# Performance work log

Measured on AMD Instinct MI355X. Metric: run time of the kernel, lower is better.

Reference implementation:

```python
import jax, jax.numpy as jnp
import numpy as np

# --- Cl(3,0,1) projective geometric algebra structure constants (GATr blade order) ---
BLADES = [(), (0,), (1,), (2,), (3,), (0, 1), (0, 2), (0, 3), (1, 2), (1, 3), (2, 3),
          (0, 1, 2), (0, 1, 3), (0, 2, 3), (1, 2, 3), (0, 1, 2, 3)]
IDX = {b: i for i, b in enumerate(BLADES)}
METRIC = [0.0, 1.0, 1.0, 1.0]  # e0 degenerate, e1,e2,e3 square to +1


def _mul_blades(a, b):
    """Multiply two basis blades; returns (sign, sorted_blade_tuple)."""
    lst = list(a) + list(b)
    sign = 1.0
    changed = True
    while changed:
        changed = False
        k = 0
        while k < len(lst) - 1:
            if lst[k] > lst[k + 1]:
                lst[k], lst[k + 1] = lst[k + 1], lst[k]
                sign = -sign
                changed = True
            elif lst[k] == lst[k + 1]:
                sign *= METRIC[lst[k]]
                del lst[k:k + 2]
                changed = True
            else:
                k += 1
    return sign, tuple(lst)


def _tables():
    gp = np.zeros((16, 16, 16), np.float32)
    outer = np.zeros((16, 16, 16), np.float32)
    for j, bj in enumerate(BLADES):
        for k, bk in enumerate(BLADES):
            s, bl = _mul_blades(bj, bk)
            if s != 0.0:
                gp[IDX[bl], j, k] = s
            if set(bj).isdisjoint(bk):  # outer product: nonzero only for disjoint blades
                outer[IDX[bl], j, k] = s
    # dual map D: blade -> signed complement, with blade ^ complement = sign * e0123
    D = np.zeros((16, 16), np.float32)
    for j, bj in enumerate(BLADES):
        comp = tuple(i for i in range(4) if i not in bj)
        s, _ = _mul_blades(bj, comp)
        D[IDX[comp], j] = s
    # join(x, y) = dual(dual(x) ^ dual(y))  ->  bilinear tensor [16,16,16]
    join = np.einsum('ai,ijk,jb,kc->abc', D, outer, D, D).astype(np.float32)
    # Pin-equivariant linear basis: 5 grade projections + 4 e0-wedge-per-grade maps
    grades = np.array([len(b) for b in BLADES])
    basis = np.zeros((9, 16, 16), np.float32)
    for g in range(5):
        basis[g] = np.diag((grades == g).astype(np.float32))
    e0_mul = outer[:, IDX[(0,)], :]  # x -> e0 ^ x
    for g in range(4):
        basis[5 + g] = e0_mul * (grades == g)[None, :].astype(np.float32)
    return gp, join, basis


B, N = 8, 4096
IN_MV, HID, OUT_MV = 32, 32, 32
HALF = HID // 2
IN_S, OUT_S = 64, 64
NB = 9


def setup_inputs() -> dict:
    key = jax.random.key(0)
    ks = jax.random.split(key, 16)
    gp, jn, basis = _tables()

    def wmv(k, o, i):
        return jax.random.normal(k, (o, i, NB), jnp.float32) / np.sqrt(i * NB)

    def ws(k, o, i):
        return jax.random.normal(k, (o, i), jnp.float32) / np.sqrt(i)

    return dict(
        multivectors=jax.random.normal(ks[0], (B, N, IN_MV, 16), jnp.float32),
        reference_mv=jax.random.normal(ks[1], (B, N, 16), jnp.float32),
        scalars=jax.random.normal(ks[2], (B, N, IN_S), jnp.float32),
        basis=jnp.asarray(basis), gp=jnp.asarray(gp), jn=jnp.asarray(jn),
        w_left_mv=wmv(ks[3], HALF, IN_MV), w_left_s=ws(ks[4], HALF, IN_S),
        w_right_mv=wmv(ks[5], HALF, IN_MV), w_right_s=ws(ks[6], HALF, IN_S),
        w_jl_mv=wmv(ks[7], HALF, IN_MV), w_jl_s=ws(ks[8], HALF, IN_S),
        w_jr_mv=wmv(ks[9], HALF, IN_MV), w_jr_s=ws(ks[10], HALF, IN_S),
        w_out_mv=wmv(ks[11], OUT_MV, HID), w_out_s2mv=ws(ks[12], OUT_MV, IN_S),
        w_out_mvs2s=ws(ks[13], OUT_S, HID), w_out_s2s=ws(ks[14], OUT_S, IN_S),
    )


def _equi_linear(x, s, w_mv, w_s, basis):
    # fold the 9 equivariant basis maps into the channel-mixing weight once (tiny)
    W = jnp.einsum('oib,bjk->oijk', w_mv, basis)  # [out, in, 16, 16]
    out = jnp.einsum('oijk,...ik->...oj', W, x)   # (..., out, 16)
    # scalar inputs feed the multivector scalar component (blade index 0)
    out = out.at[..., 0].add(jnp.einsum('os,...s->...o', w_s, s))
    return out


def reference(multivectors, reference_mv, scalars, basis, gp, jn,
              w_left_mv, w_left_s, w_right_mv, w_right_s, w_jl_mv, w_jl_s,
              w_jr_mv, w_jr_s, w_out_mv, w_out_s2mv, w_out_mvs2s, w_out_s2s):
    left = _equi_linear(multivectors, scalars, w_left_mv, w_left_s, basis)
    right = _equi_linear(multivectors, scalars, w_right_mv, w_right_s, basis)
    gp_out = jnp.einsum('ijk,...cj,...ck->...ci', gp, left, right)  # geometric product

    jl = _equi_linear(multivectors, scalars, w_jl_mv, w_jl_s, basis)
    jr = _equi_linear(multivectors, scalars, w_jr_mv, w_jr_s, basis)
    # equivariant join, scaled by pseudoscalar (e0123) component of the reference
    join_out = jnp.einsum('ijk,...cj,...ck->...ci', jn, jl, jr) * reference_mv[..., None, 15:16]

    hidden = jnp.concatenate([gp_out, join_out], axis=-2)  # (..., HID, 16)
    out_mv = _equi_linear(hidden, scalars, w_out_mv, w_out_s2mv, basis)
    out_s = jnp.einsum('oc,...c->...o', w_out_mvs2s, hidden[..., 0]) \
        + jnp.einsum('os,...s->...o', w_out_s2s, scalars)
    return out_mv, out_s
```

## Files before the change

### kernel.cpp

```cpp
#include <hip/hip_runtime.h>
#include <stdint.h>


#define NPOS_TOTAL 32768

typedef __attribute__((ext_vector_type(8))) short short8;
typedef __attribute__((ext_vector_type(4))) float f32x4;
#define MFMA16(a,b,c) __builtin_amdgcn_mfma_f32_16x16x32_bf16((a),(b),(c),0,0,0)

constexpr int BLADE_MASK[16] = {0,1,2,4,8,3,5,9,6,10,12,7,11,13,14,15};
constexpr int MASK2IDX[16]   = {0,1,2,5,3,6,8,11,4,7,9,12,10,13,14,15};

struct MulRes { int sign; int mask; };

constexpr MulRes mul_blades(int ma, int mb) {
  int lst[8] = {0,0,0,0,0,0,0,0};
  int n = 0;
  for (int g = 0; g < 4; ++g) if ((ma >> g) & 1) lst[n++] = g;
  for (int g = 0; g < 4; ++g) if ((mb >> g) & 1) lst[n++] = g;
  int sign = 1;
  bool changed = true;
  while (changed) {
    changed = false;
    int k = 0;
    while (k + 1 < n) {
      if (lst[k] > lst[k+1]) {
        int t = lst[k]; lst[k] = lst[k+1]; lst[k+1] = t;
        sign = -sign; changed = true;
      } else if (lst[k] == lst[k+1]) {
        if (lst[k] == 0) sign = 0;
        for (int m = k; m + 2 < n; ++m) lst[m] = lst[m+2];
        n -= 2; changed = true;
      } else {
        ++k;
      }
    }
  }
  int mask = 0;
  for (int m = 0; m < n; ++m) mask |= (1 << lst[m]);
  if (sign == 0) mask = 0;
  return MulRes{sign, mask};
}

struct Tables {
  float gp_sgn[16][16]; int gp_idx[16][16];
  float jn_sgn[16][16]; int jn_idx[16][16];
  constexpr Tables() : gp_sgn{}, gp_idx{}, jn_sgn{}, jn_idx{} {
    for (int j = 0; j < 16; ++j) {
      for (int k = 0; k < 16; ++k) {
        MulRes r = mul_blades(BLADE_MASK[j], BLADE_MASK[k]);
        gp_sgn[j][k] = (float)r.sign;
        gp_idx[j][k] = MASK2IDX[r.mask & 15];
        jn_sgn[j][k] = 0.0f; jn_idx[j][k] = 0;
        int mb = BLADE_MASK[j], mc = BLADE_MASK[k];
        if ((mb | mc) == 15) {
          int cb = 15 ^ mb, cc = 15 ^ mc;
          MulRes sb = mul_blades(mb, cb);
          MulRes sc = mul_blades(mc, cc);
          MulRes ro = mul_blades(cb, cc);
          int imask = ro.mask;
          int amask = 15 ^ imask;
          MulRes si = mul_blades(imask, amask);
          jn_sgn[j][k] = (float)(si.sign * ro.sign * sb.sign * sc.sign);
          jn_idx[j][k] = MASK2IDX[amask & 15];
        }
      }
    }
  }
};
constexpr Tables TBL{};

constexpr int GRADE[16] = {0,1,1,1,1,2,2,2,2,2,2,3,3,3,3,4};
constexpr int E0_TGT[8]  = {1,5,6,7,11,12,13,15};
constexpr int E0_SRC[8]  = {0,2,3,4,8,9,10,14};
constexpr int E0_SLOT[8] = {5,6,6,6,7,7,7,8};

__device__ __forceinline__ float bflo(unsigned u) { return __uint_as_float(u << 16); }
__device__ __forceinline__ float bfhi(unsigned u) { return __uint_as_float(u & 0xffff0000u); }
__device__ __forceinline__ unsigned pk2(float a, float b) {
  unsigned ua = __float_as_uint(a), ub = __float_as_uint(b);
  unsigned ra = (ua + 0x7fffu + ((ua >> 16) & 1u)) >> 16;
  unsigned rb = (ub + 0x7fffu + ((ub >> 16) & 1u)) >> 16;
  return (ra & 0xffffu) | ((rb & 0xffffu) << 16);
}
__device__ __forceinline__ unsigned short bf1(float a) {
  unsigned ua = __float_as_uint(a);
  return (unsigned short)((ua + 0x7fffu + ((ua >> 16) & 1u)) >> 16);
}

__global__ void gb_prep(const float* __restrict__ wlmv, const float* __restrict__ wrmv,
                        const float* __restrict__ wjlmv, const float* __restrict__ wjrmv,
                        const float* __restrict__ wls,  const float* __restrict__ wrs,
                        const float* __restrict__ wjls, const float* __restrict__ wjrs,
                        const float* __restrict__ womv, const float* __restrict__ ws2mv,
                        const float* __restrict__ wm2s, const float* __restrict__ ws2s,
                        uint4* __restrict__ wpk) {
  int t = blockIdx.x * 256 + threadIdx.x;
  if (t >= 168 * 64) return;
  int blk = t >> 6, l = t & 63;
  int m = l & 15, q = l >> 4;
  float v[8];
  if (blk < 104) {
    int mat = blk >> 2, ot = blk & 3;
    const float* wmv[4] = {wlmv, wrmv, wjlmv, wjrmv};
    const float* wsc[4] = {wls, wrs, wjls, wjrs};
    for (int jj = 0; jj < 8; ++jj) {
      int k = q * 8 + jj;
      if (mat < 16)      v[jj] = wmv[ot][m * 288 + k * 9 + GRADE[mat]];
      else if (mat < 24) v[jj] = wmv[ot][m * 288 + k * 9 + E0_SLOT[mat - 16]];
      else               v[jj] = wsc[ot][m * 64 + (mat - 24) * 32 + k];
    }
  } else if (blk < 156) {
    int b2 = blk - 104, mat = b2 >> 1, ot = b2 & 1;
    int o = ot * 16 + m;
    for (int jj = 0; jj < 8; ++jj) {
      int k = q * 8 + jj;
      if (mat < 16)      v[jj] = womv[o * 288 + k * 9 + GRADE[mat]];
      else if (mat < 24) v[jj] = womv[o * 288 + k * 9 + E0_SLOT[mat - 16]];
      else               v[jj] = ws2mv[o * 64 + (mat - 24) * 32 + k];
    }
  } else {
    int b4 = blk - 156;
    for (int jj = 0; jj < 8; ++jj) {
      int k = q * 8 + jj;
      if (b4 < 4) { int o = b4 * 16 + m; v[jj] = wm2s[o * 32 + k]; }
      else { int half = (b4 - 4) >> 2, ot = (b4 - 4) & 3; int o = ot * 16 + m;
             v[jj] = ws2s[o * 64 + half * 32 + k]; }
    }
  }
  uint4 u;
  u.x = pk2(v[0], v[1]); u.y = pk2(v[2], v[3]);
  u.z = pk2(v[4], v[5]); u.w = pk2(v[6], v[7]);
  wpk[t] = u;
}

__global__ __launch_bounds__(256, 4) void gb_main(
    const float* __restrict__ mv, const float* __restrict__ ref,
    const float* __restrict__ s, const uint4* __restrict__ wpk,
    float* __restrict__ out_mv, float* __restrict__ out_s) {
  __shared__ __align__(16) char smem[37376];
  unsigned short* xs_e = (unsigned short*)smem;
  unsigned*       xs_w = (unsigned*)smem;
  unsigned short* hl_e = (unsigned short*)smem;
  unsigned*       yl_w = (unsigned*)smem;

  const int tid  = threadIdx.x;
  const int wave = tid >> 6, lane = tid & 63;
  const int lm = lane & 15, lq = lane >> 4;
  const int P0 = blockIdx.x * 16;

  const float rs = ref[((size_t)(P0 + (tid & 15))) * 16 + 15];

  const float4* mv4 = (const float4*)mv + (size_t)P0 * 128;
  #pragma unroll
  for (int kk = 0; kk < 4; ++kk) {
    int e = tid + kk * 256;
    int p = e >> 6, sub = e & 63, i2 = sub >> 2, jg = sub & 3;
    float4 fa = mv4[p * 128 + i2 * 8 + jg];
    float4 fb = mv4[p * 128 + i2 * 8 + 4 + jg];
    int base = p * 260 + jg * 4 * 16 + i2;
    xs_w[base + 0 * 16] = pk2(fa.x, fb.x);
    xs_w[base + 1 * 16] = pk2(fa.y, fb.y);
    xs_w[base + 2 * 16] = pk2(fa.z, fb.z);
    xs_w[base + 3 * 16] = pk2(fa.w, fb.w);
  }

  short8 sfrag[2];
  {
    const float4* s4 = (const float4*)s + ((size_t)(P0 + lm)) * 16;
    #pragma unroll
    for (int h = 0; h < 2; ++h) {
      float4 a = s4[h * 8 + lq * 2];
      float4 b = s4[h * 8 + lq * 2 + 1];
      uint4 u;
      u.x = pk2(a.x, a.y); u.y = pk2(a.z, a.w);
      u.z = pk2(b.x, b.y); u.w = pk2(b.z, b.w);
      sfrag[h] = __builtin_bit_cast(short8, u);
    }
  }
  __syncthreads();

  {
    short8 bx[16];
    #pragma unroll
    for (int c = 0; c < 16; ++c)
      bx[c] = *(const short8*)&xs_e[lm * 520 + c * 32 + lq * 8];
    __syncthreads();
    f32x4 zf = {0.f, 0.f, 0.f, 0.f};
    f32x4 acc[16];
    #pragma unroll
    for (int j = 0; j < 16; ++j) acc[j] = zf;
    #pragma unroll
    for (int j = 0; j < 16; ++j) {
      short8 w = __builtin_bit_cast(short8, wpk[(j * 4 + wave) * 64 + lane]);
      acc[j] = MFMA16(w, bx[j], acc[j]);
    }
    #pragma unroll
    for (int m = 0; m < 8; ++m) {
      short8 w = __builtin_bit_cast(short8, wpk[((16 + m) * 4 + wave) * 64 + lane]);
      acc[E0_TGT[m]] = MFMA16(w, bx[E0_SRC[m]], acc[E0_TGT[m]]);
    }
    #pragma unroll
    for (int h = 0; h < 2; ++h) {
      short8 w = __builtin_bit_cast(short8, wpk[((24 + h) * 4 + wave) * 64 + lane]);
      acc[0] = MFMA16(w, sfrag[h], acc[0]);
    }
    #pragma unroll
    for (int jp = 0; jp < 8; ++jp) {
      #pragma unroll
      for (int r = 0; r < 4; ++r) {
        int o = wave * 16 + lq * 4 + r;
        yl_w[o * 146 + lm * 9 + jp] = pk2(acc[2 * jp][r], acc[2 * jp + 1][r]);
      }
    }
  }
  __syncthreads();

  {
    const int pos = tid & 15;
    const int hc  = tid >> 4;
    unsigned uL[8], uR[8];
    {
      const unsigned* pL = yl_w + hc * 146 + pos * 9;
      const unsigned* pR = yl_w + (16 + hc) * 146 + pos * 9;
      #pragma unroll
      for (int q = 0; q < 8; ++q) uL[q] = pL[q];
      #pragma unroll
      for (int q = 0; q < 8; ++q) uR[q] = pR[q];
    }
    __syncthreads();
    float L[16], R[16], H[16];
    #pragma unroll
    for (int q = 0; q < 8; ++q) {
      L[2*q] = bflo(uL[q]); L[2*q+1] = bfhi(uL[q]);
      R[2*q] = bflo(uR[q]); R[2*q+1] = bfhi(uR[q]);
    }
    #pragma unroll
    for (int q = 0; q < 16; ++q) H[q] = 0.f;
    #pragma unroll
    for (int j = 0; j < 16; ++j)
      #pragma unroll
      for (int k = 0; k < 16; ++k)
        if (TBL.gp_sgn[j][k] != 0.0f)
          H[TBL.gp_idx[j][k]] += TBL.gp_sgn[j][k] * L[j] * R[k];
    #pragma unroll
    for (int j = 0; j < 16; ++j)
      hl_e[pos * 520 + j * 32 + hc] = bf1(H[j]);
    {
      const unsigned* pJ = yl_w + (32 + hc) * 146 + pos * 9;
      const unsigned* pK = yl_w + (48 + hc) * 146 + pos * 9;
      #pragma unroll
      for (int q = 0; q < 8; ++q) {
        unsigned a = pJ[q];
        L[2*q] = bflo(a) * rs; L[2*q+1] = bfhi(a) * rs;
      }
      #pragma unroll
      for (int q = 0; q < 8; ++q) {
        unsigned a = pK[q];
        R[2*q] = bflo(a); R[2*q+1] = bfhi(a);
      }
    }
    #pragma unroll
    for (int q = 0; q < 16; ++q) H[q] = 0.f;
    #pragma unroll
    for (int j = 0; j < 16; ++j)
      #pragma unroll
      for (int k = 0; k < 16; ++k)
        if (TBL.jn_sgn[j][k] != 0.0f)
          H[TBL.jn_idx[j][k]] += TBL.jn_sgn[j][k] * L[j] * R[k];
    #pragma unroll
    for (int j = 0; j < 16; ++j)
      hl_e[pos * 520 + j * 32 + 16 + hc] = bf1(H[j]);
  }
  __syncthreads();

  if (wave < 2) {
    short8 bh[16];
    #pragma unroll
    for (int j = 0; j < 16; ++j)
      bh[j] = *(const short8*)&hl_e[lm * 520 + j * 32 + lq * 8];
    f32x4 zf = {0.f, 0.f, 0.f, 0.f};
    f32x4 a3[16];
    #pragma unroll
    for (int j = 0; j < 16; ++j) a3[j] = zf;
    #pragma unroll
    for (int j = 0; j < 16; ++j) {
      short8 w = __builtin_bit_cast(short8, wpk[(104 + j * 2 + wave) * 64 + lane]);
      a3[j] = MFMA16(w, bh[j], a3[j]);
    }
    #pragma unroll
    for (int m = 0; m < 8; ++m) {
      short8 w = __builtin_bit_cast(short8, wpk[(104 + (16 + m) * 2 + wave) * 64 + lane]);
      a3[E0_TGT[m]] = MFMA16(w, bh[E0_SRC[m]], a3[E0_TGT[m]]);
    }
    #pragma unroll
    for (int h = 0; h < 2; ++h) {
      short8 w = __builtin_bit_cast(short8, wpk[(104 + (24 + h) * 2 + wave) * 64 + lane]);
      a3[0] = MFMA16(w, sfrag[h], a3[0]);
    }
    float* ob = out_mv + ((size_t)(P0 + lm)) * 512 + (size_t)(wave * 16 + lq * 4) * 16;
    #pragma unroll
    for (int r = 0; r < 4; ++r) {
      #pragma unroll
      for (int g = 0; g < 4; ++g) {
        *(float4*)(ob + r * 16 + g * 4) =
            make_float4(a3[4*g][r], a3[4*g+1][r], a3[4*g+2][r], a3[4*g+3][r]);
      }
    }
  } else {
    short8 bh0 = *(const short8*)&hl_e[lm * 520 + lq * 8];
    int w2 = wave - 2;
    f32x4 zf = {0.f, 0.f, 0.f, 0.f};
    #pragma unroll
    for (int t2 = 0; t2 < 2; ++t2) {
      int otg = w2 * 2 + t2;
      f32x4 aS = zf;
      aS = MFMA16(__builtin_bit_cast(short8, wpk[(156 + otg) * 64 + lane]), bh0, aS);
      aS = MFMA16(__builtin_bit_cast(short8, wpk[(160 + otg) * 64 + lane]), sfrag[0], aS);
      aS = MFMA16(__builtin_bit_cast(short8, wpk[(164 + otg) * 64 + lane]), sfrag[1], aS);
      float* osb = out_s + ((size_t)(P0 + lm)) * 64 + otg * 16 + lq * 4;
      *(float4*)osb = make_float4(aS[0], aS[1], aS[2], aS[3]);
    }
  }
}

extern "C" void kernel_launch(void* const* d_in, const int* in_sizes, int n_in,
                              void* d_out, int out_size, void* d_ws, size_t ws_size,
                              hipStream_t stream) {
  (void)in_sizes; (void)n_in; (void)out_size; (void)ws_size;
  const float* mv    = (const float*)d_in[0];
  const float* ref   = (const float*)d_in[1];
  const float* s     = (const float*)d_in[2];
  const float* wlmv  = (const float*)d_in[6];
  const float* wls   = (const float*)d_in[7];
  const float* wrmv  = (const float*)d_in[8];
  const float* wrs   = (const float*)d_in[9];
  const float* wjlmv = (const float*)d_in[10];
  const float* wjls  = (const float*)d_in[11];
  const float* wjrmv = (const float*)d_in[12];
  const float* wjrs  = (const float*)d_in[13];
  const float* womv  = (const float*)d_in[14];
  const float* ws2mv = (const float*)d_in[15];
  const float* wm2s  = (const float*)d_in[16];
  const float* ws2s  = (const float*)d_in[17];

  float* out_mv = (float*)d_out;
  float* out_s  = out_mv + (size_t)NPOS_TOTAL * 32 * 16;
  uint4* wpk = (uint4*)d_ws;

  gb_prep<<<42, 256, 0, stream>>>(wlmv, wrmv, wjlmv, wjrmv, wls, wrs, wjls, wjrs,
                                  womv, ws2mv, wm2s, ws2s, wpk);
  gb_main<<<NPOS_TOTAL / 16, 256, 0, stream>>>(mv, ref, s, wpk, out_mv, out_s);
}
```

Baseline: 194.6 us.

## Deduplicate packed weights by grade slot and prefetch them early, separating LDS regions

The weight packing stores one fragment per unique grade/e0 slot (9 per operand) instead of one per blade, which shrinks the packed weight buffer. The main kernel loads these fragments into registers at kernel start and before the final barrier, so their latency overlaps the input staging. The y buffer moves to its own LDS region, which lets two __syncthreads be removed. In exchange, LDS use grows and launch bounds drop to 2 blocks per CU, which may lower occupancy and raise register pressure.

```diff
diff --git a/kernel.cpp b/kernel.cpp
--- a/kernel.cpp
+++ b/kernel.cpp
@@ -96,36 +96,50 @@
                         const float* __restrict__ wm2s, const float* __restrict__ ws2s,
                         uint4* __restrict__ wpk) {
   int t = blockIdx.x * 256 + threadIdx.x;
-  if (t >= 168 * 64) return;
+  if (t >= 78 * 64) return;
   int blk = t >> 6, l = t & 63;
   int m = l & 15, q = l >> 4;
   float v[8];
-  if (blk < 104) {
-    int mat = blk >> 2, ot = blk & 3;
+  if (blk < 36) {
+    int slot = blk >> 2, ot = blk & 3;
     const float* wmv[4] = {wlmv, wrmv, wjlmv, wjrmv};
+    for (int jj = 0; jj < 8; ++jj) {
+      int k = q * 8 + jj;
+      v[jj] = wmv[ot][m * 288 + k * 9 + slot];
+    }
+  } else if (blk < 44) {
+    int b = blk - 36, h = b >> 2, ot = b & 3;
     const float* wsc[4] = {wls, wrs, wjls, wjrs};
     for (int jj = 0; jj < 8; ++jj) {
       int k = q * 8 + jj;
-      if (mat < 16)      v[jj] = wmv[ot][m * 288 + k * 9 + GRADE[mat]];
-      else if (mat < 24) v[jj] = wmv[ot][m * 288 + k * 9 + E0_SLOT[mat - 16]];
-      else               v[jj] = wsc[ot][m * 64 + (mat - 24) * 32 + k];
-    }
-  } else if (blk < 156) {
-    int b2 = blk - 104, mat = b2 >> 1, ot = b2 & 1;
+      v[jj] = wsc[ot][m * 64 + h * 32 + k];
+    }
+  } else if (blk < 62) {
+    int b = blk - 44, slot = b >> 1, ot = b & 1;
     int o = ot * 16 + m;
     for (int jj = 0; jj < 8; ++jj) {
       int k = q * 8 + jj;
-      if (mat < 16)      v[jj] = womv[o * 288 + k * 9 + GRADE[mat]];
-      else if (mat < 24) v[jj] = womv[o * 288 + k * 9 + E0_SLOT[mat - 16]];
-      else               v[jj] = ws2mv[o * 64 + (mat - 24) * 32 + k];
+      v[jj] = womv[o * 288 + k * 9 + slot];
+    }
+  } else if (blk < 66) {
+    int b = blk - 62, h = b >> 1, ot = b & 1;
+    int o = ot * 16 + m;
+    for (int jj = 0; jj < 8; ++jj) {
+      int k = q * 8 + jj;
+      v[jj] = ws2mv[o * 64 + h * 32 + k];
+    }
+  } else if (blk < 70) {
+    int ot = blk - 66, o = ot * 16 + m;
+    for (int jj = 0; jj < 8; ++jj) {
+      int k = q * 8 + jj;
+      v[jj] = wm2s[o * 32 + k];
     }
   } else {
-    int b4 = blk - 156;
-    for (int jj = 0; jj < 8; ++jj) {
-      int k = q * 8 + jj;
-      if (b4 < 4) { int o = b4 * 16 + m; v[jj] = wm2s[o * 32 + k]; }
-      else { int half = (b4 - 4) >> 2, ot = (b4 - 4) & 3; int o = ot * 16 + m;
-             v[jj] = ws2s[o * 64 + half * 32 + k]; }
+    int b = blk - 70, half = b >> 2, ot = b & 3;
+    int o = ot * 16 + m;
+    for (int jj = 0; jj < 8; ++jj) {
+      int k = q * 8 + jj;
+      v[jj] = ws2s[o * 64 + half * 32 + k];
     }
   }
   uint4 u;
@@ -134,20 +148,25 @@
   wpk[t] = u;
 }
 
-__global__ __launch_bounds__(256, 4) void gb_main(
+__global__ __launch_bounds__(256, 2) void gb_main(
     const float* __restrict__ mv, const float* __restrict__ ref,
     const float* __restrict__ s, const uint4* __restrict__ wpk,
     float* __restrict__ out_mv, float* __restrict__ out_s) {
-  __shared__ __align__(16) char smem[37376];
+  __shared__ __align__(16) char smem[54016];
   unsigned short* xs_e = (unsigned short*)smem;
   unsigned*       xs_w = (unsigned*)smem;
   unsigned short* hl_e = (unsigned short*)smem;
-  unsigned*       yl_w = (unsigned*)smem;
+  unsigned*       yl_w = (unsigned*)(smem + 16640);
 
   const int tid  = threadIdx.x;
   const int wave = tid >> 6, lane = tid & 63;
   const int lm = lane & 15, lq = lane >> 4;
   const int P0 = blockIdx.x * 16;
+
+  short8 wg[5];
+  #pragma unroll
+  for (int g = 0; g < 5; ++g)
+    wg[g] = __builtin_bit_cast(short8, wpk[(g * 4 + wave) * 64 + lane]);
 
   const float rs = ref[((size_t)(P0 + (tid & 15))) * 16 + 15];
 
@@ -185,26 +204,28 @@
     #pragma unroll
     for (int c = 0; c < 16; ++c)
       bx[c] = *(const short8*)&xs_e[lm * 520 + c * 32 + lq * 8];
-    __syncthreads();
+    short8 we[4];
+    #pragma unroll
+    for (int sidx = 0; sidx < 4; ++sidx)
+      we[sidx] = __builtin_bit_cast(short8, wpk[((5 + sidx) * 4 + wave) * 64 + lane]);
+    short8 wsc1[2];
+    #pragma unroll
+    for (int h = 0; h < 2; ++h)
+      wsc1[h] = __builtin_bit_cast(short8, wpk[(36 + h * 4 + wave) * 64 + lane]);
+
     f32x4 zf = {0.f, 0.f, 0.f, 0.f};
     f32x4 acc[16];
     #pragma unroll
     for (int j = 0; j < 16; ++j) acc[j] = zf;
     #pragma unroll
-    for (int j = 0; j < 16; ++j) {
-      short8 w = __builtin_bit_cast(short8, wpk[(j * 4 + wave) * 64 + lane]);
-      acc[j] = MFMA16(w, bx[j], acc[j]);
-    }
-    #pragma unroll
-    for (int m = 0; m < 8; ++m) {
-      short8 w = __builtin_bit_cast(short8, wpk[((16 + m) * 4 + wave) * 64 + lane]);
-      acc[E0_TGT[m]] = MFMA16(w, bx[E0_SRC[m]], acc[E0_TGT[m]]);
-    }
-    #pragma unroll
-    for (int h = 0; h < 2; ++h) {
-      short8 w = __builtin_bit_cast(short8, wpk[((24 + h) * 4 + wave) * 64 + lane]);
-      acc[0] = MFMA16(w, sfrag[h], acc[0]);
-    }
+    for (int j = 0; j < 16; ++j)
+      acc[j] = MFMA16(wg[GRADE[j]], bx[j], acc[j]);
+    #pragma unroll
+    for (int m = 0; m < 8; ++m)
+      acc[E0_TGT[m]] = MFMA16(we[E0_SLOT[m] - 5], bx[E0_SRC[m]], acc[E0_TGT[m]]);
+    #pragma unroll
+    for (int h = 0; h < 2; ++h)
+      acc[0] = MFMA16(wsc1[h], sfrag[h], acc[0]);
     #pragma unroll
     for (int jp = 0; jp < 8; ++jp) {
       #pragma unroll
@@ -219,21 +240,16 @@
   {
     const int pos = tid & 15;
     const int hc  = tid >> 4;
-    unsigned uL[8], uR[8];
+    float L[16], R[16], H[16];
     {
       const unsigned* pL = yl_w + hc * 146 + pos * 9;
       const unsigned* pR = yl_w + (16 + hc) * 146 + pos * 9;
       #pragma unroll
-      for (int q = 0; q < 8; ++q) uL[q] = pL[q];
-      #pragma unroll
-      for (int q = 0; q < 8; ++q) uR[q] = pR[q];
-    }
-    __syncthreads();
-    float L[16], R[16], H[16];
-    #pragma unroll
-    for (int q = 0; q < 8; ++q) {
-      L[2*q] = bflo(uL[q]); L[2*q+1] = bfhi(uL[q]);
-      R[2*q] = bflo(uR[q]); R[2*q+1] = bfhi(uR[q]);
+      for (int q = 0; q < 8; ++q) {
+        unsigned a = pL[q], b = pR[q];
+        L[2*q] = bflo(a); L[2*q+1] = bfhi(a);
+        R[2*q] = bflo(b); R[2*q+1] = bfhi(b);
+      }
     }
     #pragma unroll
     for (int q = 0; q < 16; ++q) H[q] = 0.f;
@@ -272,6 +288,25 @@
     for (int j = 0; j < 16; ++j)
       hl_e[pos * 520 + j * 32 + 16 + hc] = bf1(H[j]);
   }
+
+  short8 w3[11];
+  if (wave < 2) {
+    #pragma unroll
+    for (int g = 0; g < 9; ++g)
+      w3[g] = __builtin_bit_cast(short8, wpk[(44 + g * 2 + wave) * 64 + lane]);
+    #pragma unroll
+    for (int h = 0; h < 2; ++h)
+      w3[9 + h] = __builtin_bit_cast(short8, wpk[(62 + h * 2 + wave) * 64 + lane]);
+  } else {
+    int w2 = wave - 2;
+    #pragma unroll
+    for (int t2 = 0; t2 < 2; ++t2) {
+      int otg = w2 * 2 + t2;
+      w3[t2 * 3 + 0] = __builtin_bit_cast(short8, wpk[(66 + otg) * 64 + lane]);
+      w3[t2 * 3 + 1] = __builtin_bit_cast(short8, wpk[(70 + otg) * 64 + lane]);
+      w3[t2 * 3 + 2] = __builtin_bit_cast(short8, wpk[(74 + otg) * 64 + lane]);
+    }
+  }
   __syncthreads();
 
   if (wave < 2) {
@@ -284,20 +319,14 @@
     #pragma unroll
     for (int j = 0; j < 16; ++j) a3[j] = zf;
     #pragma unroll
-    for (int j = 0; j < 16; ++j) {
-      short8 w = __builtin_bit_cast(short8, wpk[(104 + j * 2 + wave) * 64 + lane]);
-      a3[j] = MFMA16(w, bh[j], a3[j]);
-    }
-    #pragma unroll
-    for (int m = 0; m < 8; ++m) {
-      short8 w = __builtin_bit_cast(short8, wpk[(104 + (16 + m) * 2 + wave) * 64 + lane]);
-      a3[E0_TGT[m]] = MFMA16(w, bh[E0_SRC[m]], a3[E0_TGT[m]]);
-    }
-    #pragma unroll
-    for (int h = 0; h < 2; ++h) {
-      short8 w = __builtin_bit_cast(short8, wpk[(104 + (24 + h) * 2 + wave) * 64 + lane]);
-      a3[0] = MFMA16(w, sfrag[h], a3[0]);
-    }
+    for (int j = 0; j < 16; ++j)
+      a3[j] = MFMA16(w3[GRADE[j]], bh[j], a3[j]);
+    #pragma unroll
+    for (int m = 0; m < 8; ++m)
+      a3[E0_TGT[m]] = MFMA16(w3[E0_SLOT[m]], bh[E0_SRC[m]], a3[E0_TGT[m]]);
+    #pragma unroll
+    for (int h = 0; h < 2; ++h)
+      a3[0] = MFMA16(w3[9 + h], sfrag[h], a3[0]);
     float* ob = out_mv + ((size_t)(P0 + lm)) * 512 + (size_t)(wave * 16 + lq * 4) * 16;
     #pragma unroll
     for (int r = 0; r < 4; ++r) {
@@ -309,15 +338,14 @@
     }
   } else {
     short8 bh0 = *(const short8*)&hl_e[lm * 520 + lq * 8];
-    int w2 = wave - 2;
     f32x4 zf = {0.f, 0.f, 0.f, 0.f};
     #pragma unroll
     for (int t2 = 0; t2 < 2; ++t2) {
-      int otg = w2 * 2 + t2;
+      int otg = (wave - 2) * 2 + t2;
       f32x4 aS = zf;
-      aS = MFMA16(__builtin_bit_cast(short8, wpk[(156 + otg) * 64 + lane]), bh0, aS);
-      aS = MFMA16(__builtin_bit_cast(short8, wpk[(160 + otg) * 64 + lane]), sfrag[0], aS);
-      aS = MFMA16(__builtin_bit_cast(short8, wpk[(164 + otg) * 64 + lane]), sfrag[1], aS);
+      aS = MFMA16(w3[t2 * 3 + 0], bh0, aS);
+      aS = MFMA16(w3[t2 * 3 + 1], sfrag[0], aS);
+      aS = MFMA16(w3[t2 * 3 + 2], sfrag[1], aS);
       float* osb = out_s + ((size_t)(P0 + lm)) * 64 + otg * 16 + lq * 4;
       *(float4*)osb = make_float4(aS[0], aS[1], aS[2], aS[3]);
     }
@@ -348,7 +376,7 @@
   float* out_s  = out_mv + (size_t)NPOS_TOTAL * 32 * 16;
   uint4* wpk = (uint4*)d_ws;
 
-  gb_prep<<<42, 256, 0, stream>>>(wlmv, wrmv, wjlmv, wjrmv, wls, wrs, wjls, wjrs,
+  gb_prep<<<20, 256, 0, stream>>>(wlmv, wrmv, wjlmv, wjrmv, wls, wrs, wjls, wjrs,
                                   womv, ws2mv, wm2s, ws2s, wpk);
   gb_main<<<NPOS_TOTAL / 16, 256, 0, stream>>>(mv, ref, s, wpk, out_mv, out_s);
 }
```

Measured after the change: 186.1 us. 4.4% less time.
